# Performance work log

Hardware: AMD Instinct MI355X
Metric: run time of the kernel (lower is better)

## Reference

```python
import jax, jax.numpy as jnp
import numpy as np

B, M, D = 16, 16, 512          # m (tokens per sample) must equal num_experts
N = 16                          # num_experts
H = (D + D) * 2 // 3            # hidden_dim = 682
OUT = 512


def setup_inputs() -> dict:
    key = jax.random.key(0)
    ks = jax.random.split(key, 8)
    s = lambda k, shape, fan: jax.random.normal(k, shape, jnp.float32) / np.sqrt(fan)
    return {
        "x":    jax.random.normal(ks[0], (B, M, D), jnp.float32),
        "phi":  jax.random.normal(ks[1], (D, N, H), jnp.float32),
        "W1":   s(ks[2], (N, D, H), D),
        "b1":   s(ks[3], (N, H), D),
        "W2":   s(ks[4], (N, H, D), H),
        "b2":   s(ks[5], (N, D), H),
        "Wout": s(ks[6], (N * D, OUT), N * D),
        "bout": s(ks[7], (OUT,), N * D),
    }


def reference(x, phi, W1, b1, W2, b2, Wout, bout):
    # dispatch/combine logits: [b, m, n, p]
    logits = jnp.einsum('bmd,dnp->bmnp', x, phi)
    Dw = jax.nn.softmax(logits, axis=1)                       # dispatch weights over tokens m
    Cw = jax.nn.softmax(jax.nn.softmax(logits, axis=2), axis=3)  # (softmax of softmax, faithful)
    Xs = jnp.einsum('bmd,bmnp->bnpd', x, Dw)                  # expert slot inputs [b,n,p,d]
    # batched per-expert MLP (grouped GEMM over expert axis n)
    hmid = jax.nn.relu(jnp.einsum('bnpd,ndh->bnph', Xs, W1) + b1[None, :, None, :])
    Ys = jnp.einsum('bnph,nhd->bnpd', hmid, W2) + b2[None, :, None, :]
    Y = jnp.einsum('bnpd,bmnp->bmd', Ys, Cw)                  # combine -> [b, m, d]
    flat = Y.reshape(Y.shape[0], -1)                          # [b, m*d] == [b, n*d]
    return flat @ Wout + bout
```

## Files before the change

kernel.cpp:

```cpp
#include <hip/hip_runtime.h>
#include <hip/hip_bf16.h>
#include <math.h>

typedef unsigned int   u32;
typedef unsigned short u16;
typedef __bf16 bf16;
typedef bf16  bf16x8  __attribute__((ext_vector_type(8)));
typedef float f32x4   __attribute__((ext_vector_type(4)));
typedef float f32x16  __attribute__((ext_vector_type(16)));

#define BBATCH 16
#define MTOK   16
#define NEXP   16
#define DDIM   512
#define HDIM   682
#define HPAD   704
#define NHCOL  (NEXP*HDIM)
#define NHPCOL (NEXP*HPAD)
#define BM     (BBATCH*MTOK)

__device__ __forceinline__ u16 f2bf(float f) {
    u32 u = __builtin_bit_cast(u32, f);
    u += 0x7fffu + ((u >> 16) & 1u);
    return (u16)(u >> 16);
}
__device__ __forceinline__ float bf2f(u16 h) {
    u32 u = ((u32)h) << 16;
    return __builtin_bit_cast(float, u);
}
__device__ __forceinline__ u32 pk2bf(float a, float b) {
    __hip_bfloat162 t = __float22bfloat162_rn(float2{a, b});
    u32 r;
    __builtin_memcpy(&r, &t, 4);
    return r;
}

__global__ __launch_bounds__(256) void k_prep(
    const float* __restrict__ x, const float* __restrict__ b2,
    const float* __restrict__ bout,
    u16* __restrict__ xh, u16* __restrict__ xl,
    float* __restrict__ Y, float* __restrict__ out, u16* __restrict__ DwT) {
    const int bid = blockIdx.x, tid = threadIdx.x;
    if (bid < 128) {
        int i = (bid * 256 + tid) * 4;
        float4 v = *(const float4*)&x[i];
        float a[4] = {v.x, v.y, v.z, v.w};
        u16 hh[4], ll[4];
        #pragma unroll
        for (int j = 0; j < 4; ++j) {
            hh[j] = f2bf(a[j]);
            ll[j] = f2bf(a[j] - bf2f(hh[j]));
        }
        *(uint2*)&xh[i] = make_uint2((u32)hh[0] | ((u32)hh[1] << 16), (u32)hh[2] | ((u32)hh[3] << 16));
        *(uint2*)&xl[i] = make_uint2((u32)ll[0] | ((u32)ll[1] << 16), (u32)ll[2] | ((u32)ll[3] << 16));
    } else if (bid < 640) {
        int idx = (bid - 128) * 256 + tid;
        int d = idx & 511;
        float s = 0.f;
        #pragma unroll
        for (int nn = 0; nn < 16; ++nn) s += b2[nn * 512 + d];
        Y[idx] = s;
    } else if (bid < 672) {
        int idx = (bid - 640) * 256 + tid;
        out[idx] = bout[idx & 511];
    } else {
        int g = (bid - 672) * 256 + tid;
        int bn = g / 88, off = g - bn * 88;
        *(uint2*)(DwT + (size_t)(bn * HPAD + HDIM) * 16 + off * 4) = make_uint2(0u, 0u);
    }
}

__global__ __launch_bounds__(256) void k_lgemm(
    const u16* __restrict__ xh, const u16* __restrict__ xl,
    const float* __restrict__ phi, float* __restrict__ C,
    u16* __restrict__ DwT) {
    __shared__ u16 AH[128 * 40], AL[128 * 40], BH[64 * 40], BL[64 * 40];
    __shared__ float F[32 * 68];
    const int ct = blockIdx.x, rt = blockIdx.y;
    const int tid = threadIdx.x;
    const int wv = tid >> 6, lane = tid & 63, quad = lane >> 4, l15 = lane & 15;
    f32x4 acc[2][4] = {};
    for (int kb = 0; kb < 512; kb += 32) {
        {
            int rr = tid >> 2, kg = (tid & 3) * 8;
            #pragma unroll
            for (int rp = 0; rp < 2; ++rp) {
                int r = rp * 64 + rr;
                size_t ao = (size_t)(rt * 128 + r) * 512 + kb + kg;
                *(uint4*)&AH[r * 40 + kg] = *(const uint4*)(xh + ao);
                *(uint4*)&AL[r * 40 + kg] = *(const uint4*)(xl + ao);
            }
        }
        {
            int dl = tid >> 3, cg = (tid & 7) * 8;
            int c0 = ct * 64 + cg;
            const float* src = phi + (size_t)(kb + dl) * NHCOL + c0;
            float v[8];
            if (c0 + 8 <= NHCOL) {
                *(float4*)&v[0] = *(const float4*)&src[0];
                *(float4*)&v[4] = *(const float4*)&src[4];
            } else {
                #pragma unroll
                for (int i = 0; i < 8; ++i) v[i] = (c0 + i < NHCOL) ? src[i] : 0.f;
            }
            #pragma unroll
            for (int i = 0; i < 8; ++i) F[dl * 68 + cg + i] = v[i];
        }
        __syncthreads();
        {
            int cc = tid & 63, q = tid >> 6;
            u16 th[8], tl[8];
            #pragma unroll
            for (int i = 0; i < 8; ++i) {
                float v = F[(q * 8 + i) * 68 + cc];
                th[i] = f2bf(v);
                tl[i] = f2bf(v - bf2f(th[i]));
            }
            *(uint4*)&BH[cc * 40 + q * 8] = *(uint4*)&th[0];
            *(uint4*)&BL[cc * 40 + q * 8] = *(uint4*)&tl[0];
        }
        __syncthreads();
        bf16x8 ah[2], al[2];
        #pragma unroll
        for (int i = 0; i < 2; ++i) {
            ah[i] = *(const bf16x8*)&AH[(wv * 32 + i * 16 + l15) * 40 + quad * 8];
            al[i] = *(const bf16x8*)&AL[(wv * 32 + i * 16 + l15) * 40 + quad * 8];
        }
        #pragma unroll
        for (int j = 0; j < 4; ++j) {
            bf16x8 bh = *(const bf16x8*)&BH[(j * 16 + l15) * 40 + quad * 8];
            bf16x8 bl = *(const bf16x8*)&BL[(j * 16 + l15) * 40 + quad * 8];
            #pragma unroll
            for (int i = 0; i < 2; ++i) {
                acc[i][j] = __builtin_amdgcn_mfma_f32_16x16x32_bf16(ah[i], bh, acc[i][j], 0, 0, 0);
                acc[i][j] = __builtin_amdgcn_mfma_f32_16x16x32_bf16(ah[i], bl, acc[i][j], 0, 0, 0);
                acc[i][j] = __builtin_amdgcn_mfma_f32_16x16x32_bf16(al[i], bh, acc[i][j], 0, 0, 0);
            }
        }
        __syncthreads();
    }
    #pragma unroll
    for (int i = 0; i < 2; ++i) {
        const int b  = rt * 8 + wv * 2 + i;
        const int r0 = rt * 128 + wv * 32 + i * 16 + quad * 4;
        #pragma unroll
        for (int j = 0; j < 4; ++j) {
            const int col = ct * 64 + j * 16 + l15;
            float a0 = acc[i][j][0], a1 = acc[i][j][1], a2 = acc[i][j][2], a3 = acc[i][j][3];
            if (col < NHCOL) {
                C[(size_t)(r0 + 0) * NHCOL + col] = a0;
                C[(size_t)(r0 + 1) * NHCOL + col] = a1;
                C[(size_t)(r0 + 2) * NHCOL + col] = a2;
                C[(size_t)(r0 + 3) * NHCOL + col] = a3;
            }
            float mx = fmaxf(fmaxf(a0, a1), fmaxf(a2, a3));
            mx = fmaxf(mx, __shfl_xor(mx, 16));
            mx = fmaxf(mx, __shfl_xor(mx, 32));
            float e0 = expf(a0 - mx), e1 = expf(a1 - mx);
            float e2 = expf(a2 - mx), e3 = expf(a3 - mx);
            float s = e0 + e1 + e2 + e3;
            s += __shfl_xor(s, 16);
            s += __shfl_xor(s, 32);
            float inv = 1.f / s;
            if (col < NHCOL) {
                int n = col / HDIM;
                int p = col - n * HDIM;
                u16* dst = DwT + ((size_t)((b * 16 + n) * HPAD + p)) * 16 + quad * 4;
                *(uint2*)dst = make_uint2(pk2bf(e0 * inv, e1 * inv), pk2bf(e2 * inv, e3 * inv));
            }
        }
    }
}

__global__ __launch_bounds__(256) void k_t1cw(
    const u16* __restrict__ A, const float* __restrict__ W1,
    u16* __restrict__ T1b,
    const float* __restrict__ L, u16* __restrict__ CwB) {
    __shared__ __align__(16) char smem[NHCOL * 4];
    const int bid = blockIdx.x, tid = threadIdx.x;
    if (bid < 176) {
        u16*   As = (u16*)smem;
        u16*   Bs = (u16*)(smem + 20480);
        float* F  = (float*)(smem + 25600);
        const int ct = bid;
        const int wv = tid >> 6, lane = tid & 63, quad = lane >> 4, l15 = lane & 15;
        const int n = ct / 11, h0 = (ct % 11) * 64;
        f32x4 acc[4][4] = {};
        for (int kb = 0; kb < 512; kb += 32) {
            {
                int rr = tid >> 2, kg = (tid & 3) * 8;
                #pragma unroll
                for (int rp = 0; rp < 4; ++rp) {
                    int r = rp * 64 + rr;
                    *(uint4*)&As[r * 40 + kg] = *(const uint4*)(A + (size_t)r * 512 + kb + kg);
                }
            }
            {
                int dl = tid >> 3, cg = (tid & 7) * 8;
                int h = h0 + cg;
                const float* wr = W1 + ((size_t)n * 512 + kb + dl) * HDIM + h;
                float v[8];
                if (h + 8 <= HDIM) {
                    #pragma unroll
                    for (int i = 0; i < 4; ++i) {
                        float2 t = *(const float2*)&wr[i * 2];
                        v[i * 2] = t.x; v[i * 2 + 1] = t.y;
                    }
                } else {
                    #pragma unroll
                    for (int i = 0; i < 8; ++i) v[i] = (h + i < HDIM) ? wr[i] : 0.f;
                }
                #pragma unroll
                for (int i = 0; i < 8; ++i) F[dl * 68 + cg + i] = v[i];
            }
            __syncthreads();
            {
                int cc = tid & 63, q = tid >> 6;
                u16 tv[8];
                #pragma unroll
                for (int i = 0; i < 8; ++i) tv[i] = f2bf(F[(q * 8 + i) * 68 + cc]);
                *(uint4*)&Bs[cc * 40 + q * 8] = *(uint4*)&tv[0];
            }
            __syncthreads();
            bf16x8 af[4], bfr[4];
            #pragma unroll
            for (int i = 0; i < 4; ++i)
                af[i] = *(const bf16x8*)&As[(wv * 64 + i * 16 + l15) * 40 + quad * 8];
            #pragma unroll
            for (int j = 0; j < 4; ++j)
                bfr[j] = *(const bf16x8*)&Bs[(j * 16 + l15) * 40 + quad * 8];
            #pragma unroll
            for (int i = 0; i < 4; ++i)
                #pragma unroll
                for (int j = 0; j < 4; ++j)
                    acc[i][j] = __builtin_amdgcn_mfma_f32_16x16x32_bf16(af[i], bfr[j], acc[i][j], 0, 0, 0);
            __syncthreads();
        }
        #pragma unroll
        for (int i = 0; i < 4; ++i)
            #pragma unroll
            for (int j = 0; j < 4; ++j) {
                int col = ct * 64 + j * 16 + l15;
                int r0  = wv * 64 + i * 16 + quad * 4;
                #pragma unroll
                for (int r = 0; r < 4; ++r)
                    T1b[(size_t)(r0 + r) * NHPCOL + col] = f2bf(acc[i][j][r]);
            }
    } else {
        float* row = (float*)smem;
        const int j = bid - 176;
        const int m = j & 15, b = j >> 4;
        const float* Lrow = L + (size_t)(b * 16 + m) * NHCOL;
        for (int i = tid; i < NHCOL; i += 256) row[i] = Lrow[i];
        __syncthreads();
        for (int p = tid; p < HDIM; p += 256) {
            float v[16];
            float mx = -1e30f;
            #pragma unroll
            for (int n = 0; n < 16; ++n) { v[n] = row[n * HDIM + p]; mx = fmaxf(mx, v[n]); }
            float s = 0.f;
            #pragma unroll
            for (int n = 0; n < 16; ++n) { v[n] = expf(v[n] - mx); s += v[n]; }
            float inv = 1.f / s;
            #pragma unroll
            for (int n = 0; n < 16; ++n) row[n * HDIM + p] = expf(v[n] * inv);
        }
        __syncthreads();
        const int wv = tid >> 6, lane = tid & 63;
        for (int nn = 0; nn < 4; ++nn) {
            int n = wv * 4 + nn;
            float s = 0.f;
            for (int p = lane; p < HDIM; p += 64) s += row[n * HDIM + p];
            #pragma unroll
            for (int off = 32; off > 0; off >>= 1) s += __shfl_xor(s, off);
            float inv = 1.f / s;
            u16* dst = CwB + (size_t)(((b * 16 + n) * 16 + m)) * HPAD;
            for (int p = lane; p < HDIM; p += 64) dst[p] = f2bf(row[n * HDIM + p] * inv);
            if (lane < HPAD - HDIM) dst[HDIM + lane] = 0;
        }
    }
}

__global__ __launch_bounds__(256) void k_mid(
    const u16* __restrict__ T1b, const u16* __restrict__ DwT,
    const u16* __restrict__ CwB, const float* __restrict__ b1,
    u16* __restrict__ Gb) {
    __shared__ u16 T1T[128 * 24];
    __shared__ u16 hmidT[128 * 64];
    const int ht = blockIdx.x, n = blockIdx.y, b = blockIdx.z;
    const int tid = threadIdx.x;
    const int wv = tid >> 6, lane = tid & 63;
    const int quad = lane >> 4, l15 = lane & 15;
    const int l31 = lane & 31, half = lane >> 5;
    const int h0 = ht * 128;
    const int b16n = b * 16 + n;

    {
        int m = tid & 15, hh0 = (tid >> 4) * 8;
        u16 v[8];
        if (h0 + hh0 + 8 <= HPAD) {
            *(uint4*)v = *(const uint4*)(T1b + (size_t)(b * 16 + m) * NHPCOL + n * HPAD + h0 + hh0);
        } else {
            #pragma unroll
            for (int i = 0; i < 8; ++i) v[i] = 0;
        }
        #pragma unroll
        for (int i = 0; i < 8; ++i) T1T[(hh0 + i) * 24 + m] = v[i];
    }
    __syncthreads();

    const int hrow = wv * 32 + l31;
    bf16x8 bt1 = *(const bf16x8*)&T1T[hrow * 24 + half * 8];
    int hg1 = h0 + hrow;
    float biasf = (hg1 < HDIM) ? b1[n * HDIM + hg1] : 0.f;
    f32x16 cbias;
    #pragma unroll
    for (int i = 0; i < 16; ++i) cbias[i] = biasf;

    const u16* dwbase = DwT + (size_t)(b16n * HPAD) * 16;
    const u16* cwrow  = CwB + (size_t)(b16n * 16 + l15) * HPAD;

    f32x4 acc[2] = {};
    const int hsw = hrow & 7;
    for (int c = 0; c < 11; ++c) {
        const int p0 = c * 64;
        #pragma unroll
        for (int pt = 0; pt < 2; ++pt) {
            bf16x8 adw = *(const bf16x8*)(dwbase + (size_t)(p0 + pt * 32 + l31) * 16 + half * 8);
            f32x16 hm = __builtin_amdgcn_mfma_f32_32x32x16_bf16(adw, bt1, cbias, 0, 0, 0);
            #pragma unroll
            for (int g = 0; g < 4; ++g) {
                float v0 = fmaxf(hm[g * 4 + 0], 0.f);
                float v1 = fmaxf(hm[g * 4 + 1], 0.f);
                float v2 = fmaxf(hm[g * 4 + 2], 0.f);
                float v3 = fmaxf(hm[g * 4 + 3], 0.f);
                uint2 pk = make_uint2(pk2bf(v0, v1), pk2bf(v2, v3));
                int gran = (pt * 4 + g) ^ hsw;
                *(uint2*)&hmidT[hrow * 64 + gran * 8 + half * 4] = pk;
            }
        }
        #pragma unroll
        for (int s = 0; s < 2; ++s) {
            bf16x8 acw = *(const bf16x8*)(cwrow + p0 + s * 32 + quad * 8);
            #pragma unroll
            for (int hj = 0; hj < 2; ++hj) {
                int hr = wv * 32 + hj * 16 + l15;
                int gr = (s * 4 + quad) ^ (hr & 7);
                bf16x8 bh = *(const bf16x8*)&hmidT[hr * 64 + gr * 8];
                acc[hj] = __builtin_amdgcn_mfma_f32_16x16x32_bf16(acw, bh, acc[hj], 0, 0, 0);
            }
        }
    }
    #pragma unroll
    for (int hj = 0; hj < 2; ++hj) {
        int h = h0 + wv * 32 + hj * 16 + l15;
        if (h < HPAD) {
            #pragma unroll
            for (int r = 0; r < 4; ++r) {
                int m = quad * 4 + r;
                Gb[(size_t)(b * 16 + m) * NHPCOL + n * HPAD + h] = f2bf(acc[hj][r]);
            }
        }
    }
}

__global__ __launch_bounds__(256) void k_ygemm(
    const u16* __restrict__ G, const float* __restrict__ W2, float* __restrict__ Y) {
    __shared__ u16 AsL[64 * 40];
    __shared__ u16 BsL[128 * 40];
    __shared__ float F[32 * 132];
    const int ct = blockIdx.x, rt = blockIdx.y, nz = blockIdx.z;
    const int n = nz >> 1, kb0 = (nz & 1) * 352;
    const int tid = threadIdx.x;
    const int wv = tid >> 6, lane = tid & 63, quad = lane >> 4, l15 = lane & 15;
    const int m0 = rt * 64, d0 = ct * 128;
    f32x4 acc[4][2] = {};
    for (int kb = kb0; kb < kb0 + 352; kb += 32) {
        {
            int am = tid >> 2, akg = (tid & 3) * 8;
            *(uint4*)&AsL[am * 40 + akg] =
                *(const uint4*)(G + (size_t)(m0 + am) * NHPCOL + n * HPAD + kb + akg);
        }
        {
            int hl = tid >> 3, cg = (tid & 7) * 16;
            int h = kb + hl;
            float v[16];
            if (h < HDIM) {
                const float* src = W2 + ((size_t)n * HDIM + h) * 512 + d0 + cg;
                *(float4*)&v[0]  = *(const float4*)&src[0];
                *(float4*)&v[4]  = *(const float4*)&src[4];
                *(float4*)&v[8]  = *(const float4*)&src[8];
                *(float4*)&v[12] = *(const float4*)&src[12];
            } else {
                #pragma unroll
                for (int i = 0; i < 16; ++i) v[i] = 0.f;
            }
            #pragma unroll
            for (int i = 0; i < 16; ++i) F[hl * 132 + cg + i] = v[i];
        }
        __syncthreads();
        {
            int cc = tid & 127, half = tid >> 7;
            u16 tv[16];
            #pragma unroll
            for (int i = 0; i < 16; ++i) tv[i] = f2bf(F[(half * 16 + i) * 132 + cc]);
            *(uint4*)&BsL[cc * 40 + half * 16]     = *(uint4*)&tv[0];
            *(uint4*)&BsL[cc * 40 + half * 16 + 8] = *(uint4*)&tv[8];
        }
        __syncthreads();
        bf16x8 af[4], bfr[2];
        #pragma unroll
        for (int i = 0; i < 4; ++i) af[i] = *(const bf16x8*)&AsL[(i * 16 + l15) * 40 + quad * 8];
        #pragma unroll
        for (int j = 0; j < 2; ++j) bfr[j] = *(const bf16x8*)&BsL[(wv * 32 + j * 16 + l15) * 40 + quad * 8];
        #pragma unroll
        for (int i = 0; i < 4; ++i)
            #pragma unroll
            for (int j = 0; j < 2; ++j)
                acc[i][j] = __builtin_amdgcn_mfma_f32_16x16x32_bf16(af[i], bfr[j], acc[i][j], 0, 0, 0);
        __syncthreads();
    }
    #pragma unroll
    for (int i = 0; i < 4; ++i)
        #pragma unroll
        for (int j = 0; j < 2; ++j) {
            int d = d0 + wv * 32 + j * 16 + l15;
            int r0 = m0 + i * 16 + quad * 4;
            #pragma unroll
            for (int r = 0; r < 4; ++r)
                atomicAdd(&Y[(size_t)(r0 + r) * 512 + d], acc[i][j][r]);
        }
}

__global__ __launch_bounds__(256) void k_outgemm(
    const float* __restrict__ Y, const float* __restrict__ Wout, float* __restrict__ out) {
    __shared__ u16 AsL[16 * 40];
    __shared__ u16 BsL[128 * 40];
    __shared__ float F[32 * 132];
    const int ct = blockIdx.x, ks = blockIdx.y;
    const int tid = threadIdx.x;
    const int wv = tid >> 6, lane = tid & 63, quad = lane >> 4, l15 = lane & 15;
    const int o0 = ct * 128, kbase = ks * 128;
    f32x4 acc[2] = {};
    for (int kb = 0; kb < 128; kb += 32) {
        {
            int r = tid >> 4, k2 = (tid & 15) * 2;
            float2 v = *(const float2*)&Y[(size_t)r * 8192 + kbase + kb + k2];
            AsL[r * 40 + k2]     = f2bf(v.x);
            AsL[r * 40 + k2 + 1] = f2bf(v.y);
        }
        {
            int kl = tid >> 3, cg = (tid & 7) * 16;
            const float* src = Wout + (size_t)(kbase + kb + kl) * 512 + o0 + cg;
            float v[16];
            *(float4*)&v[0]  = *(const float4*)&src[0];
            *(float4*)&v[4]  = *(const float4*)&src[4];
            *(float4*)&v[8]  = *(const float4*)&src[8];
            *(float4*)&v[12] = *(const float4*)&src[12];
            #pragma unroll
            for (int i = 0; i < 16; ++i) F[kl * 132 + cg + i] = v[i];
        }
        __syncthreads();
        {
            int cc = tid & 127, half = tid >> 7;
            u16 tv[16];
            #pragma unroll
            for (int i = 0; i < 16; ++i) tv[i] = f2bf(F[(half * 16 + i) * 132 + cc]);
            *(uint4*)&BsL[cc * 40 + half * 16]     = *(uint4*)&tv[0];
            *(uint4*)&BsL[cc * 40 + half * 16 + 8] = *(uint4*)&tv[8];
        }
        __syncthreads();
        bf16x8 af = *(const bf16x8*)&AsL[l15 * 40 + quad * 8];
        #pragma unroll
        for (int j = 0; j < 2; ++j) {
            bf16x8 bfr = *(const bf16x8*)&BsL[(wv * 32 + j * 16 + l15) * 40 + quad * 8];
            acc[j] = __builtin_amdgcn_mfma_f32_16x16x32_bf16(af, bfr, acc[j], 0, 0, 0);
        }
        __syncthreads();
    }
    #pragma unroll
    for (int j = 0; j < 2; ++j) {
        int o = o0 + wv * 32 + j * 16 + l15;
        #pragma unroll
        for (int r = 0; r < 4; ++r)
            atomicAdd(&out[(size_t)(quad * 4 + r) * 512 + o], acc[j][r]);
    }
}

extern "C" void kernel_launch(void* const* d_in, const int* in_sizes, int n_in,
                              void* d_out, int out_size, void* d_ws, size_t ws_size,
                              hipStream_t stream) {
    const float* x    = (const float*)d_in[0];
    const float* phi  = (const float*)d_in[1];
    const float* W1   = (const float*)d_in[2];
    const float* b1   = (const float*)d_in[3];
    const float* W2   = (const float*)d_in[4];
    const float* b2   = (const float*)d_in[5];
    const float* Wout = (const float*)d_in[6];
    const float* bout = (const float*)d_in[7];
    float* out = (float*)d_out;

    char* base = (char*)d_ws;
    float* logits = (float*)(base + 0);
    u16*   DwT    = (u16*)(base + 11173888);
    u16*   CwB    = (u16*)(base + 16941056);
    u16*   T1b    = (u16*)(base + 22708224);
    u16*   Gb     = (u16*)(base + 28475392);
    u16*   xh     = (u16*)(base + 34242560);
    u16*   xl     = (u16*)(base + 34504704);
    float* Y      = (float*)(base + 34766848);

    k_prep    <<<dim3(760), 256, 0, stream>>>(x, b2, bout, xh, xl, Y, out, DwT);
    k_lgemm   <<<dim3(171, 2), 256, 0, stream>>>(xh, xl, phi, logits, DwT);
    k_t1cw    <<<dim3(432), 256, 0, stream>>>(xh, W1, T1b, logits, CwB);
    k_mid     <<<dim3(6, 16, 16), 256, 0, stream>>>(T1b, DwT, CwB, b1, Gb);
    k_ygemm   <<<dim3(4, 4, 32), 256, 0, stream>>>(Gb, W2, Y);
    k_outgemm <<<dim3(4, 64), 256, 0, stream>>>(Y, Wout, out);
}
```

Baseline: 233.9 us.

## Fuse all stages into one persistent kernel with grid barriers and ticket scheduling

Six separate kernel launches are replaced by a single persistent kernel of 512 blocks. Each stage pulls work items through an atomic ticket counter, and stages are separated by software grid barriers built on atomics. Several stages are also re-tiled into smaller pieces: the logits GEMM uses 64-row tiles, the T1 GEMM is split into row halves, and the output GEMM has a finer K split. The aim is to remove launch gaps and tail idling between kernels, at the cost of barrier spin overhead, a memset launch, and a deadlock risk if the 512 blocks cannot all be resident at once. The barrier has a timeout guard that silently breaks out, which could produce incorrect results.

```diff
diff --git a/kernel.cpp b/kernel.cpp
--- a/kernel.cpp
+++ b/kernel.cpp
@@ -17,7 +17,7 @@
 #define HPAD   704
 #define NHCOL  (NEXP*HDIM)
 #define NHPCOL (NEXP*HPAD)
-#define BM     (BBATCH*MTOK)
+#define NBLK   512
 
 __device__ __forceinline__ u16 f2bf(float f) {
     u32 u = __builtin_bit_cast(u32, f);
@@ -35,222 +35,246 @@
     return r;
 }
 
-__global__ __launch_bounds__(256) void k_prep(
-    const float* __restrict__ x, const float* __restrict__ b2,
-    const float* __restrict__ bout,
-    u16* __restrict__ xh, u16* __restrict__ xl,
-    float* __restrict__ Y, float* __restrict__ out, u16* __restrict__ DwT) {
-    const int bid = blockIdx.x, tid = threadIdx.x;
-    if (bid < 128) {
-        int i = (bid * 256 + tid) * 4;
-        float4 v = *(const float4*)&x[i];
-        float a[4] = {v.x, v.y, v.z, v.w};
-        u16 hh[4], ll[4];
-        #pragma unroll
-        for (int j = 0; j < 4; ++j) {
-            hh[j] = f2bf(a[j]);
-            ll[j] = f2bf(a[j] - bf2f(hh[j]));
-        }
-        *(uint2*)&xh[i] = make_uint2((u32)hh[0] | ((u32)hh[1] << 16), (u32)hh[2] | ((u32)hh[3] << 16));
-        *(uint2*)&xl[i] = make_uint2((u32)ll[0] | ((u32)ll[1] << 16), (u32)ll[2] | ((u32)ll[3] << 16));
-    } else if (bid < 640) {
-        int idx = (bid - 128) * 256 + tid;
-        int d = idx & 511;
-        float s = 0.f;
-        #pragma unroll
-        for (int nn = 0; nn < 16; ++nn) s += b2[nn * 512 + d];
-        Y[idx] = s;
-    } else if (bid < 672) {
-        int idx = (bid - 640) * 256 + tid;
-        out[idx] = bout[idx & 511];
-    } else {
-        int g = (bid - 672) * 256 + tid;
-        int bn = g / 88, off = g - bn * 88;
-        *(uint2*)(DwT + (size_t)(bn * HPAD + HDIM) * 16 + off * 4) = make_uint2(0u, 0u);
-    }
+__device__ __forceinline__ void gridbar(u32* cnt, u32* gen, u32 k) {
+    __threadfence();
+    __syncthreads();
+    if (threadIdx.x == 0) {
+        u32 old = __hip_atomic_fetch_add(cnt, 1u, __ATOMIC_RELAXED, __HIP_MEMORY_SCOPE_AGENT);
+        if (old == k * (u32)NBLK - 1u) {
+            __hip_atomic_fetch_add(gen, 1u, __ATOMIC_RELEASE, __HIP_MEMORY_SCOPE_AGENT);
+        } else {
+            long long guard = 0;
+            while (__hip_atomic_load(gen, __ATOMIC_RELAXED, __HIP_MEMORY_SCOPE_AGENT) < k) {
+                __builtin_amdgcn_s_sleep(8);
+                if (++guard > (1LL << 21)) break;
+            }
+        }
+    }
+    __syncthreads();
+    __threadfence();
 }
 
-__global__ __launch_bounds__(256) void k_lgemm(
-    const u16* __restrict__ xh, const u16* __restrict__ xl,
-    const float* __restrict__ phi, float* __restrict__ C,
-    u16* __restrict__ DwT) {
-    __shared__ u16 AH[128 * 40], AL[128 * 40], BH[64 * 40], BL[64 * 40];
-    __shared__ float F[32 * 68];
-    const int ct = blockIdx.x, rt = blockIdx.y;
+__global__ __launch_bounds__(256, 2) void k_moe(
+    const float* __restrict__ x,    const float* __restrict__ phi,
+    const float* __restrict__ W1,   const float* __restrict__ b1,
+    const float* __restrict__ W2,   const float* __restrict__ b2,
+    const float* __restrict__ Wout, const float* __restrict__ bout,
+    float* __restrict__ out,
+    float* __restrict__ logits, u16* __restrict__ DwT, u16* __restrict__ CwB,
+    u16* __restrict__ T1b, u16* __restrict__ Gb,
+    u16* __restrict__ xh, u16* __restrict__ xl, float* __restrict__ Y,
+    u32* __restrict__ ctl) {
+
+    __shared__ __align__(16) char SMEM[43648];
+    __shared__ u32 sh_vb;
+    u32* tk  = ctl;
+    u32* cnt = ctl + 6;
+    u32* gen = ctl + 7;
     const int tid = threadIdx.x;
     const int wv = tid >> 6, lane = tid & 63, quad = lane >> 4, l15 = lane & 15;
-    f32x4 acc[2][4] = {};
-    for (int kb = 0; kb < 512; kb += 32) {
-        {
-            int rr = tid >> 2, kg = (tid & 3) * 8;
-            #pragma unroll
-            for (int rp = 0; rp < 2; ++rp) {
-                int r = rp * 64 + rr;
-                size_t ao = (size_t)(rt * 128 + r) * 512 + kb + kg;
-                *(uint4*)&AH[r * 40 + kg] = *(const uint4*)(xh + ao);
-                *(uint4*)&AL[r * 40 + kg] = *(const uint4*)(xl + ao);
-            }
-        }
-        {
-            int dl = tid >> 3, cg = (tid & 7) * 8;
-            int c0 = ct * 64 + cg;
-            const float* src = phi + (size_t)(kb + dl) * NHCOL + c0;
-            float v[8];
-            if (c0 + 8 <= NHCOL) {
-                *(float4*)&v[0] = *(const float4*)&src[0];
-                *(float4*)&v[4] = *(const float4*)&src[4];
-            } else {
-                #pragma unroll
-                for (int i = 0; i < 8; ++i) v[i] = (c0 + i < NHCOL) ? src[i] : 0.f;
-            }
-            #pragma unroll
-            for (int i = 0; i < 8; ++i) F[dl * 68 + cg + i] = v[i];
-        }
-        __syncthreads();
-        {
-            int cc = tid & 63, q = tid >> 6;
-            u16 th[8], tl[8];
-            #pragma unroll
-            for (int i = 0; i < 8; ++i) {
-                float v = F[(q * 8 + i) * 68 + cc];
-                th[i] = f2bf(v);
-                tl[i] = f2bf(v - bf2f(th[i]));
-            }
-            *(uint4*)&BH[cc * 40 + q * 8] = *(uint4*)&th[0];
-            *(uint4*)&BL[cc * 40 + q * 8] = *(uint4*)&tl[0];
-        }
-        __syncthreads();
-        bf16x8 ah[2], al[2];
-        #pragma unroll
-        for (int i = 0; i < 2; ++i) {
-            ah[i] = *(const bf16x8*)&AH[(wv * 32 + i * 16 + l15) * 40 + quad * 8];
-            al[i] = *(const bf16x8*)&AL[(wv * 32 + i * 16 + l15) * 40 + quad * 8];
-        }
-        #pragma unroll
-        for (int j = 0; j < 4; ++j) {
-            bf16x8 bh = *(const bf16x8*)&BH[(j * 16 + l15) * 40 + quad * 8];
-            bf16x8 bl = *(const bf16x8*)&BL[(j * 16 + l15) * 40 + quad * 8];
-            #pragma unroll
-            for (int i = 0; i < 2; ++i) {
-                acc[i][j] = __builtin_amdgcn_mfma_f32_16x16x32_bf16(ah[i], bh, acc[i][j], 0, 0, 0);
-                acc[i][j] = __builtin_amdgcn_mfma_f32_16x16x32_bf16(ah[i], bl, acc[i][j], 0, 0, 0);
-                acc[i][j] = __builtin_amdgcn_mfma_f32_16x16x32_bf16(al[i], bh, acc[i][j], 0, 0, 0);
-            }
-        }
-        __syncthreads();
-    }
-    #pragma unroll
-    for (int i = 0; i < 2; ++i) {
-        const int b  = rt * 8 + wv * 2 + i;
-        const int r0 = rt * 128 + wv * 32 + i * 16 + quad * 4;
-        #pragma unroll
-        for (int j = 0; j < 4; ++j) {
-            const int col = ct * 64 + j * 16 + l15;
-            float a0 = acc[i][j][0], a1 = acc[i][j][1], a2 = acc[i][j][2], a3 = acc[i][j][3];
-            if (col < NHCOL) {
-                C[(size_t)(r0 + 0) * NHCOL + col] = a0;
-                C[(size_t)(r0 + 1) * NHCOL + col] = a1;
-                C[(size_t)(r0 + 2) * NHCOL + col] = a2;
-                C[(size_t)(r0 + 3) * NHCOL + col] = a3;
-            }
-            float mx = fmaxf(fmaxf(a0, a1), fmaxf(a2, a3));
-            mx = fmaxf(mx, __shfl_xor(mx, 16));
-            mx = fmaxf(mx, __shfl_xor(mx, 32));
-            float e0 = expf(a0 - mx), e1 = expf(a1 - mx);
-            float e2 = expf(a2 - mx), e3 = expf(a3 - mx);
-            float s = e0 + e1 + e2 + e3;
-            s += __shfl_xor(s, 16);
-            s += __shfl_xor(s, 32);
-            float inv = 1.f / s;
-            if (col < NHCOL) {
-                int n = col / HDIM;
-                int p = col - n * HDIM;
-                u16* dst = DwT + ((size_t)((b * 16 + n) * HPAD + p)) * 16 + quad * 4;
-                *(uint2*)dst = make_uint2(pk2bf(e0 * inv, e1 * inv), pk2bf(e2 * inv, e3 * inv));
-            }
-        }
-    }
-}
-
-__global__ __launch_bounds__(256) void k_t1cw(
-    const u16* __restrict__ A, const float* __restrict__ W1,
-    u16* __restrict__ T1b,
-    const float* __restrict__ L, u16* __restrict__ CwB) {
-    __shared__ __align__(16) char smem[NHCOL * 4];
-    const int bid = blockIdx.x, tid = threadIdx.x;
-    if (bid < 176) {
-        u16*   As = (u16*)smem;
-        u16*   Bs = (u16*)(smem + 20480);
-        float* F  = (float*)(smem + 25600);
-        const int ct = bid;
-        const int wv = tid >> 6, lane = tid & 63, quad = lane >> 4, l15 = lane & 15;
-        const int n = ct / 11, h0 = (ct % 11) * 64;
-        f32x4 acc[4][4] = {};
-        for (int kb = 0; kb < 512; kb += 32) {
-            {
-                int rr = tid >> 2, kg = (tid & 3) * 8;
-                #pragma unroll
-                for (int rp = 0; rp < 4; ++rp) {
-                    int r = rp * 64 + rr;
-                    *(uint4*)&As[r * 40 + kg] = *(const uint4*)(A + (size_t)r * 512 + kb + kg);
-                }
-            }
-            {
-                int dl = tid >> 3, cg = (tid & 7) * 8;
-                int h = h0 + cg;
-                const float* wr = W1 + ((size_t)n * 512 + kb + dl) * HDIM + h;
-                float v[8];
-                if (h + 8 <= HDIM) {
-                    #pragma unroll
-                    for (int i = 0; i < 4; ++i) {
-                        float2 t = *(const float2*)&wr[i * 2];
-                        v[i * 2] = t.x; v[i * 2 + 1] = t.y;
+
+#define TICKET(P, NVB)                                                         \
+    if (tid == 0) sh_vb = __hip_atomic_fetch_add(&tk[P], 1u, __ATOMIC_RELAXED, \
+                                                 __HIP_MEMORY_SCOPE_AGENT);    \
+    __syncthreads();                                                           \
+    u32 vb = sh_vb;                                                            \
+    if (vb >= (NVB)) break;
+
+    for (;;) {
+        TICKET(0, 760)
+        if (vb < 128) {
+            int i = ((int)vb * 256 + tid) * 4;
+            float4 v = *(const float4*)&x[i];
+            float a[4] = {v.x, v.y, v.z, v.w};
+            u16 hh[4], ll[4];
+            #pragma unroll
+            for (int j = 0; j < 4; ++j) {
+                hh[j] = f2bf(a[j]);
+                ll[j] = f2bf(a[j] - bf2f(hh[j]));
+            }
+            *(uint2*)&xh[i] = make_uint2((u32)hh[0] | ((u32)hh[1] << 16), (u32)hh[2] | ((u32)hh[3] << 16));
+            *(uint2*)&xl[i] = make_uint2((u32)ll[0] | ((u32)ll[1] << 16), (u32)ll[2] | ((u32)ll[3] << 16));
+        } else if (vb < 640) {
+            int idx = ((int)vb - 128) * 256 + tid;
+            int d = idx & 511;
+            float s = 0.f;
+            #pragma unroll
+            for (int nn = 0; nn < 16; ++nn) s += b2[nn * 512 + d];
+            Y[idx] = s;
+        } else if (vb < 672) {
+            int idx = ((int)vb - 640) * 256 + tid;
+            out[idx] = bout[idx & 511];
+        } else {
+            int g = ((int)vb - 672) * 256 + tid;
+            int bn = g / 88, off = g - bn * 88;
+            *(uint2*)(DwT + (size_t)(bn * HPAD + HDIM) * 16 + off * 4) = make_uint2(0u, 0u);
+        }
+        __syncthreads();
+    }
+    gridbar(cnt, gen, 1);
+
+    for (;;) {
+        TICKET(1, 1036)
+        if (vb < 684) {
+            const int ct = (int)vb % 171, rt = (int)vb / 171;
+            u16* AH = (u16*)SMEM;
+            u16* AL = (u16*)(SMEM + 5120);
+            u16* BH = (u16*)(SMEM + 10240);
+            u16* BL = (u16*)(SMEM + 15360);
+            float* F = (float*)(SMEM + 20480);
+            f32x4 acc[4] = {};
+            for (int kb = 0; kb < 512; kb += 32) {
+                {
+                    int r = tid >> 2, kg = (tid & 3) * 8;
+                    size_t ao = (size_t)(rt * 64 + r) * 512 + kb + kg;
+                    *(uint4*)&AH[r * 40 + kg] = *(const uint4*)(xh + ao);
+                    *(uint4*)&AL[r * 40 + kg] = *(const uint4*)(xl + ao);
+                }
+                {
+                    int dl = tid >> 3, cg = (tid & 7) * 8;
+                    int c0 = ct * 64 + cg;
+                    const float* src = phi + (size_t)(kb + dl) * NHCOL + c0;
+                    float v[8];
+                    if (c0 + 8 <= NHCOL) {
+                        *(float4*)&v[0] = *(const float4*)&src[0];
+                        *(float4*)&v[4] = *(const float4*)&src[4];
+                    } else {
+                        #pragma unroll
+                        for (int i = 0; i < 8; ++i) v[i] = (c0 + i < NHCOL) ? src[i] : 0.f;
                     }
-                } else {
-                    #pragma unroll
-                    for (int i = 0; i < 8; ++i) v[i] = (h + i < HDIM) ? wr[i] : 0.f;
-                }
-                #pragma unroll
-                for (int i = 0; i < 8; ++i) F[dl * 68 + cg + i] = v[i];
-            }
-            __syncthreads();
-            {
-                int cc = tid & 63, q = tid >> 6;
-                u16 tv[8];
-                #pragma unroll
-                for (int i = 0; i < 8; ++i) tv[i] = f2bf(F[(q * 8 + i) * 68 + cc]);
-                *(uint4*)&Bs[cc * 40 + q * 8] = *(uint4*)&tv[0];
-            }
-            __syncthreads();
-            bf16x8 af[4], bfr[4];
-            #pragma unroll
-            for (int i = 0; i < 4; ++i)
-                af[i] = *(const bf16x8*)&As[(wv * 64 + i * 16 + l15) * 40 + quad * 8];
-            #pragma unroll
-            for (int j = 0; j < 4; ++j)
-                bfr[j] = *(const bf16x8*)&Bs[(j * 16 + l15) * 40 + quad * 8];
-            #pragma unroll
-            for (int i = 0; i < 4; ++i)
+                    #pragma unroll
+                    for (int i = 0; i < 8; ++i) F[dl * 68 + cg + i] = v[i];
+                }
+                __syncthreads();
+                {
+                    int cc = tid & 63, q = tid >> 6;
+                    u16 th[8], tl[8];
+                    #pragma unroll
+                    for (int i = 0; i < 8; ++i) {
+                        float v = F[(q * 8 + i) * 68 + cc];
+                        th[i] = f2bf(v);
+                        tl[i] = f2bf(v - bf2f(th[i]));
+                    }
+                    *(uint4*)&BH[cc * 40 + q * 8] = *(uint4*)&th[0];
+                    *(uint4*)&BL[cc * 40 + q * 8] = *(uint4*)&tl[0];
+                }
+                __syncthreads();
+                bf16x8 ah = *(const bf16x8*)&AH[(wv * 16 + l15) * 40 + quad * 8];
+                bf16x8 al = *(const bf16x8*)&AL[(wv * 16 + l15) * 40 + quad * 8];
+                #pragma unroll
+                for (int j = 0; j < 4; ++j) {
+                    bf16x8 bh = *(const bf16x8*)&BH[(j * 16 + l15) * 40 + quad * 8];
+                    bf16x8 bl = *(const bf16x8*)&BL[(j * 16 + l15) * 40 + quad * 8];
+                    acc[j] = __builtin_amdgcn_mfma_f32_16x16x32_bf16(ah, bh, acc[j], 0, 0, 0);
+                    acc[j] = __builtin_amdgcn_mfma_f32_16x16x32_bf16(ah, bl, acc[j], 0, 0, 0);
+                    acc[j] = __builtin_amdgcn_mfma_f32_16x16x32_bf16(al, bh, acc[j], 0, 0, 0);
+                }
+                __syncthreads();
+            }
+            const int b  = rt * 4 + wv;
+            const int r0 = rt * 64 + wv * 16 + quad * 4;
+            #pragma unroll
+            for (int j = 0; j < 4; ++j) {
+                const int col = ct * 64 + j * 16 + l15;
+                float a0 = acc[j][0], a1 = acc[j][1], a2 = acc[j][2], a3 = acc[j][3];
+                if (col < NHCOL) {
+                    logits[(size_t)(r0 + 0) * NHCOL + col] = a0;
+                    logits[(size_t)(r0 + 1) * NHCOL + col] = a1;
+                    logits[(size_t)(r0 + 2) * NHCOL + col] = a2;
+                    logits[(size_t)(r0 + 3) * NHCOL + col] = a3;
+                }
+                float mx = fmaxf(fmaxf(a0, a1), fmaxf(a2, a3));
+                mx = fmaxf(mx, __shfl_xor(mx, 16));
+                mx = fmaxf(mx, __shfl_xor(mx, 32));
+                float e0 = expf(a0 - mx), e1 = expf(a1 - mx);
+                float e2 = expf(a2 - mx), e3 = expf(a3 - mx);
+                float s = e0 + e1 + e2 + e3;
+                s += __shfl_xor(s, 16);
+                s += __shfl_xor(s, 32);
+                float inv = 1.f / s;
+                if (col < NHCOL) {
+                    int n = col / HDIM;
+                    int p = col - n * HDIM;
+                    u16* dst = DwT + ((size_t)((b * 16 + n) * HPAD + p)) * 16 + quad * 4;
+                    *(uint2*)dst = make_uint2(pk2bf(e0 * inv, e1 * inv), pk2bf(e2 * inv, e3 * inv));
+                }
+            }
+        } else {
+            const int w = (int)vb - 684;
+            const int ct = w >> 1, rh = w & 1;
+            const int n = ct / 11, h0 = (ct % 11) * 64;
+            u16* As = (u16*)SMEM;
+            u16* Bs = (u16*)(SMEM + 10240);
+            float* F = (float*)(SMEM + 15360);
+            f32x4 acc[2][4] = {};
+            for (int kb = 0; kb < 512; kb += 32) {
+                {
+                    int r = tid >> 1, kg = (tid & 1) * 16;
+                    const u16* s = xh + (size_t)(rh * 128 + r) * 512 + kb + kg;
+                    *(uint4*)&As[r * 40 + kg]     = *(const uint4*)s;
+                    *(uint4*)&As[r * 40 + kg + 8] = *(const uint4*)(s + 8);
+                }
+                {
+                    int dl = tid >> 3, cg = (tid & 7) * 8;
+                    int h = h0 + cg;
+                    const float* wr = W1 + ((size_t)n * 512 + kb + dl) * HDIM + h;
+                    float v[8];
+                    if (h + 8 <= HDIM) {
+                        #pragma unroll
+                        for (int i = 0; i < 4; ++i) {
+                            float2 t = *(const float2*)&wr[i * 2];
+                            v[i * 2] = t.x; v[i * 2 + 1] = t.y;
+                        }
+                    } else {
+                        #pragma unroll
+                        for (int i = 0; i < 8; ++i) v[i] = (h + i < HDIM) ? wr[i] : 0.f;
+                    }
+                    #pragma unroll
+                    for (int i = 0; i < 8; ++i) F[dl * 68 + cg + i] = v[i];
+                }
+                __syncthreads();
+                {
+                    int cc = tid & 63, q = tid >> 6;
+                    u16 tv[8];
+                    #pragma unroll
+                    for (int i = 0; i < 8; ++i) tv[i] = f2bf(F[(q * 8 + i) * 68 + cc]);
+                    *(uint4*)&Bs[cc * 40 + q * 8] = *(uint4*)&tv[0];
+                }
+                __syncthreads();
+                bf16x8 af[2], bfr[4];
+                #pragma unroll
+                for (int i = 0; i < 2; ++i)
+                    af[i] = *(const bf16x8*)&As[(wv * 32 + i * 16 + l15) * 40 + quad * 8];
                 #pragma unroll
                 for (int j = 0; j < 4; ++j)
-                    acc[i][j] = __builtin_amdgcn_mfma_f32_16x16x32_bf16(af[i], bfr[j], acc[i][j], 0, 0, 0);
-            __syncthreads();
-        }
-        #pragma unroll
-        for (int i = 0; i < 4; ++i)
-            #pragma unroll
-            for (int j = 0; j < 4; ++j) {
-                int col = ct * 64 + j * 16 + l15;
-                int r0  = wv * 64 + i * 16 + quad * 4;
-                #pragma unroll
-                for (int r = 0; r < 4; ++r)
-                    T1b[(size_t)(r0 + r) * NHPCOL + col] = f2bf(acc[i][j][r]);
-            }
-    } else {
-        float* row = (float*)smem;
-        const int j = bid - 176;
-        const int m = j & 15, b = j >> 4;
-        const float* Lrow = L + (size_t)(b * 16 + m) * NHCOL;
+                    bfr[j] = *(const bf16x8*)&Bs[(j * 16 + l15) * 40 + quad * 8];
+                #pragma unroll
+                for (int i = 0; i < 2; ++i)
+                    #pragma unroll
+                    for (int j = 0; j < 4; ++j)
+                        acc[i][j] = __builtin_amdgcn_mfma_f32_16x16x32_bf16(af[i], bfr[j], acc[i][j], 0, 0, 0);
+                __syncthreads();
+            }
+            #pragma unroll
+            for (int i = 0; i < 2; ++i)
+                #pragma unroll
+                for (int j = 0; j < 4; ++j) {
+                    int col = ct * 64 + j * 16 + l15;
+                    int r0  = rh * 128 + wv * 32 + i * 16 + quad * 4;
+                    #pragma unroll
+                    for (int r = 0; r < 4; ++r)
+                        T1b[(size_t)(r0 + r) * NHPCOL + col] = f2bf(acc[i][j][r]);
+                }
+        }
+        __syncthreads();
+    }
+    gridbar(cnt, gen, 2);
+
+    for (;;) {
+        TICKET(2, 256)
+        float* row = (float*)SMEM;
+        const int m = (int)vb & 15, b = (int)vb >> 4;
+        const float* Lrow = logits + (size_t)(b * 16 + m) * NHCOL;
         for (int i = tid; i < NHCOL; i += 256) row[i] = Lrow[i];
         __syncthreads();
         for (int p = tid; p < HDIM; p += 256) {
@@ -266,7 +290,6 @@
             for (int n = 0; n < 16; ++n) row[n * HDIM + p] = expf(v[n] * inv);
         }
         __syncthreads();
-        const int wv = tid >> 6, lane = tid & 63;
         for (int nn = 0; nn < 4; ++nn) {
             int n = wv * 4 + nn;
             float s = 0.f;
@@ -278,213 +301,211 @@
             for (int p = lane; p < HDIM; p += 64) dst[p] = f2bf(row[n * HDIM + p] * inv);
             if (lane < HPAD - HDIM) dst[HDIM + lane] = 0;
         }
-    }
-}
-
-__global__ __launch_bounds__(256) void k_mid(
-    const u16* __restrict__ T1b, const u16* __restrict__ DwT,
-    const u16* __restrict__ CwB, const float* __restrict__ b1,
-    u16* __restrict__ Gb) {
-    __shared__ u16 T1T[128 * 24];
-    __shared__ u16 hmidT[128 * 64];
-    const int ht = blockIdx.x, n = blockIdx.y, b = blockIdx.z;
-    const int tid = threadIdx.x;
-    const int wv = tid >> 6, lane = tid & 63;
-    const int quad = lane >> 4, l15 = lane & 15;
-    const int l31 = lane & 31, half = lane >> 5;
-    const int h0 = ht * 128;
-    const int b16n = b * 16 + n;
-
-    {
-        int m = tid & 15, hh0 = (tid >> 4) * 8;
-        u16 v[8];
-        if (h0 + hh0 + 8 <= HPAD) {
-            *(uint4*)v = *(const uint4*)(T1b + (size_t)(b * 16 + m) * NHPCOL + n * HPAD + h0 + hh0);
-        } else {
-            #pragma unroll
-            for (int i = 0; i < 8; ++i) v[i] = 0;
-        }
+        __syncthreads();
+    }
+    gridbar(cnt, gen, 3);
+
+    for (;;) {
+        TICKET(3, 1536)
+        const int ht = (int)vb % 6, n = ((int)vb / 6) & 15, b = (int)vb / 96;
+        u16* T1T   = (u16*)SMEM;
+        u16* hmidT = (u16*)(SMEM + 6144);
+        const int l31 = lane & 31, half = lane >> 5;
+        const int h0 = ht * 128;
+        const int b16n = b * 16 + n;
+        {
+            int m = tid & 15, hh0 = (tid >> 4) * 8;
+            u16 v[8];
+            if (h0 + hh0 + 8 <= HPAD) {
+                *(uint4*)v = *(const uint4*)(T1b + (size_t)(b * 16 + m) * NHPCOL + n * HPAD + h0 + hh0);
+            } else {
+                #pragma unroll
+                for (int i = 0; i < 8; ++i) v[i] = 0;
+            }
+            #pragma unroll
+            for (int i = 0; i < 8; ++i) T1T[(hh0 + i) * 24 + m] = v[i];
+        }
+        __syncthreads();
+
+        const int hrow = wv * 32 + l31;
+        bf16x8 bt1 = *(const bf16x8*)&T1T[hrow * 24 + half * 8];
+        int hg1 = h0 + hrow;
+        float biasf = (hg1 < HDIM) ? b1[n * HDIM + hg1] : 0.f;
+        f32x16 cbias;
         #pragma unroll
-        for (int i = 0; i < 8; ++i) T1T[(hh0 + i) * 24 + m] = v[i];
-    }
-    __syncthreads();
-
-    const int hrow = wv * 32 + l31;
-    bf16x8 bt1 = *(const bf16x8*)&T1T[hrow * 24 + half * 8];
-    int hg1 = h0 + hrow;
-    float biasf = (hg1 < HDIM) ? b1[n * HDIM + hg1] : 0.f;
-    f32x16 cbias;
-    #pragma unroll
-    for (int i = 0; i < 16; ++i) cbias[i] = biasf;
-
-    const u16* dwbase = DwT + (size_t)(b16n * HPAD) * 16;
-    const u16* cwrow  = CwB + (size_t)(b16n * 16 + l15) * HPAD;
-
-    f32x4 acc[2] = {};
-    const int hsw = hrow & 7;
-    for (int c = 0; c < 11; ++c) {
-        const int p0 = c * 64;
+        for (int i = 0; i < 16; ++i) cbias[i] = biasf;
+
+        const u16* dwbase = DwT + (size_t)(b16n * HPAD) * 16;
+        const u16* cwrow  = CwB + (size_t)(b16n * 16 + l15) * HPAD;
+
+        f32x4 acc[2] = {};
+        const int hsw = hrow & 7;
+        for (int c = 0; c < 11; ++c) {
+            const int p0 = c * 64;
+            #pragma unroll
+            for (int pt = 0; pt < 2; ++pt) {
+                bf16x8 adw = *(const bf16x8*)(dwbase + (size_t)(p0 + pt * 32 + l31) * 16 + half * 8);
+                f32x16 hm = __builtin_amdgcn_mfma_f32_32x32x16_bf16(adw, bt1, cbias, 0, 0, 0);
+                #pragma unroll
+                for (int g = 0; g < 4; ++g) {
+                    float v0 = fmaxf(hm[g * 4 + 0], 0.f);
+                    float v1 = fmaxf(hm[g * 4 + 1], 0.f);
+                    float v2 = fmaxf(hm[g * 4 + 2], 0.f);
+                    float v3 = fmaxf(hm[g * 4 + 3], 0.f);
+                    uint2 pk = make_uint2(pk2bf(v0, v1), pk2bf(v2, v3));
+                    int gran = (pt * 4 + g) ^ hsw;
+                    *(uint2*)&hmidT[hrow * 64 + gran * 8 + half * 4] = pk;
+                }
+            }
+            #pragma unroll
+            for (int s = 0; s < 2; ++s) {
+                bf16x8 acw = *(const bf16x8*)(cwrow + p0 + s * 32 + quad * 8);
+                #pragma unroll
+                for (int hj = 0; hj < 2; ++hj) {
+                    int hr = wv * 32 + hj * 16 + l15;
+                    int gr = (s * 4 + quad) ^ (hr & 7);
+                    bf16x8 bh = *(const bf16x8*)&hmidT[hr * 64 + gr * 8];
+                    acc[hj] = __builtin_amdgcn_mfma_f32_16x16x32_bf16(acw, bh, acc[hj], 0, 0, 0);
+                }
+            }
+        }
         #pragma unroll
-        for (int pt = 0; pt < 2; ++pt) {
-            bf16x8 adw = *(const bf16x8*)(dwbase + (size_t)(p0 + pt * 32 + l31) * 16 + half * 8);
-            f32x16 hm = __builtin_amdgcn_mfma_f32_32x32x16_bf16(adw, bt1, cbias, 0, 0, 0);
-            #pragma unroll
-            for (int g = 0; g < 4; ++g) {
-                float v0 = fmaxf(hm[g * 4 + 0], 0.f);
-                float v1 = fmaxf(hm[g * 4 + 1], 0.f);
-                float v2 = fmaxf(hm[g * 4 + 2], 0.f);
-                float v3 = fmaxf(hm[g * 4 + 3], 0.f);
-                uint2 pk = make_uint2(pk2bf(v0, v1), pk2bf(v2, v3));
-                int gran = (pt * 4 + g) ^ hsw;
-                *(uint2*)&hmidT[hrow * 64 + gran * 8 + half * 4] = pk;
-            }
+        for (int hj = 0; hj < 2; ++hj) {
+            int h = h0 + wv * 32 + hj * 16 + l15;
+            if (h < HPAD) {
+                #pragma unroll
+                for (int r = 0; r < 4; ++r) {
+                    int m = quad * 4 + r;
+                    Gb[(size_t)(b * 16 + m) * NHPCOL + n * HPAD + h] = f2bf(acc[hj][r]);
+                }
+            }
+        }
+        __syncthreads();
+    }
+    gridbar(cnt, gen, 4);
+
+    for (;;) {
+        TICKET(4, 512)
+        const int ct = (int)vb & 3, rt = ((int)vb >> 2) & 3, nz = (int)vb >> 4;
+        const int n = nz >> 1, kb0 = (nz & 1) * 352;
+        u16* As = (u16*)SMEM;
+        u16* Bs = (u16*)(SMEM + 5120);
+        float* F = (float*)(SMEM + 15360);
+        const int m0 = rt * 64, d0 = ct * 128;
+        f32x4 acc[4][2] = {};
+        for (int kb = kb0; kb < kb0 + 352; kb += 32) {
+            {
+                int am = tid >> 2, akg = (tid & 3) * 8;
+                *(uint4*)&As[am * 40 + akg] =
+                    *(const uint4*)(Gb + (size_t)(m0 + am) * NHPCOL + n * HPAD + kb + akg);
+            }
+            {
+                int hl = tid >> 3, cg = (tid & 7) * 16;
+                int h = kb + hl;
+                float v[16];
+                if (h < HDIM) {
+                    const float* src = W2 + ((size_t)n * HDIM + h) * 512 + d0 + cg;
+                    *(float4*)&v[0]  = *(const float4*)&src[0];
+                    *(float4*)&v[4]  = *(const float4*)&src[4];
+                    *(float4*)&v[8]  = *(const float4*)&src[8];
+                    *(float4*)&v[12] = *(const float4*)&src[12];
+                } else {
+                    #pragma unroll
+                    for (int i = 0; i < 16; ++i) v[i] = 0.f;
+                }
+                #pragma unroll
+                for (int i = 0; i < 16; ++i) F[hl * 132 + cg + i] = v[i];
+            }
+            __syncthreads();
+            {
+                int cc = tid & 127, hf = tid >> 7;
+                u16 tv[16];
+                #pragma unroll
+                for (int i = 0; i < 16; ++i) tv[i] = f2bf(F[(hf * 16 + i) * 132 + cc]);
+                *(uint4*)&Bs[cc * 40 + hf * 16]     = *(uint4*)&tv[0];
+                *(uint4*)&Bs[cc * 40 + hf * 16 + 8] = *(uint4*)&tv[8];
+            }
+            __syncthreads();
+            bf16x8 af[4], bfr[2];
+            #pragma unroll
+            for (int i = 0; i < 4; ++i) af[i] = *(const bf16x8*)&As[(i * 16 + l15) * 40 + quad * 8];
+            #pragma unroll
+            for (int j = 0; j < 2; ++j) bfr[j] = *(const bf16x8*)&Bs[(wv * 32 + j * 16 + l15) * 40 + quad * 8];
+            #pragma unroll
+            for (int i = 0; i < 4; ++i)
+                #pragma unroll
+                for (int j = 0; j < 2; ++j)
+                    acc[i][j] = __builtin_amdgcn_mfma_f32_16x16x32_bf16(af[i], bfr[j], acc[i][j], 0, 0, 0);
+            __syncthreads();
         }
         #pragma unroll
-        for (int s = 0; s < 2; ++s) {
-            bf16x8 acw = *(const bf16x8*)(cwrow + p0 + s * 32 + quad * 8);
-            #pragma unroll
-            for (int hj = 0; hj < 2; ++hj) {
-                int hr = wv * 32 + hj * 16 + l15;
-                int gr = (s * 4 + quad) ^ (hr & 7);
-                bf16x8 bh = *(const bf16x8*)&hmidT[hr * 64 + gr * 8];
-                acc[hj] = __builtin_amdgcn_mfma_f32_16x16x32_bf16(acw, bh, acc[hj], 0, 0, 0);
-            }
-        }
-    }
-    #pragma unroll
-    for (int hj = 0; hj < 2; ++hj) {
-        int h = h0 + wv * 32 + hj * 16 + l15;
-        if (h < HPAD) {
-            #pragma unroll
-            for (int r = 0; r < 4; ++r) {
-                int m = quad * 4 + r;
-                Gb[(size_t)(b * 16 + m) * NHPCOL + n * HPAD + h] = f2bf(acc[hj][r]);
-            }
-        }
-    }
-}
-
-__global__ __launch_bounds__(256) void k_ygemm(
-    const u16* __restrict__ G, const float* __restrict__ W2, float* __restrict__ Y) {
-    __shared__ u16 AsL[64 * 40];
-    __shared__ u16 BsL[128 * 40];
-    __shared__ float F[32 * 132];
-    const int ct = blockIdx.x, rt = blockIdx.y, nz = blockIdx.z;
-    const int n = nz >> 1, kb0 = (nz & 1) * 352;
-    const int tid = threadIdx.x;
-    const int wv = tid >> 6, lane = tid & 63, quad = lane >> 4, l15 = lane & 15;
-    const int m0 = rt * 64, d0 = ct * 128;
-    f32x4 acc[4][2] = {};
-    for (int kb = kb0; kb < kb0 + 352; kb += 32) {
-        {
-            int am = tid >> 2, akg = (tid & 3) * 8;
-            *(uint4*)&AsL[am * 40 + akg] =
-                *(const uint4*)(G + (size_t)(m0 + am) * NHPCOL + n * HPAD + kb + akg);
-        }
-        {
-            int hl = tid >> 3, cg = (tid & 7) * 16;
-            int h = kb + hl;
-            float v[16];
-            if (h < HDIM) {
-                const float* src = W2 + ((size_t)n * HDIM + h) * 512 + d0 + cg;
+        for (int i = 0; i < 4; ++i)
+            #pragma unroll
+            for (int j = 0; j < 2; ++j) {
+                int d = d0 + wv * 32 + j * 16 + l15;
+                int r0 = m0 + i * 16 + quad * 4;
+                #pragma unroll
+                for (int r = 0; r < 4; ++r)
+                    atomicAdd(&Y[(size_t)(r0 + r) * 512 + d], acc[i][j][r]);
+            }
+        __syncthreads();
+    }
+    gridbar(cnt, gen, 5);
+
+    for (;;) {
+        TICKET(5, 512)
+        const int ct = (int)vb & 3, ks = (int)vb >> 2;
+        u16* As = (u16*)SMEM;
+        u16* Bs = (u16*)(SMEM + 1280);
+        float* F = (float*)(SMEM + 11520);
+        const int o0 = ct * 128, kbase = ks * 64;
+        f32x4 acc[2] = {};
+        for (int kb = 0; kb < 64; kb += 32) {
+            {
+                int r = tid >> 4, k2 = (tid & 15) * 2;
+                float2 v = *(const float2*)&Y[(size_t)r * 8192 + kbase + kb + k2];
+                As[r * 40 + k2]     = f2bf(v.x);
+                As[r * 40 + k2 + 1] = f2bf(v.y);
+            }
+            {
+                int kl = tid >> 3, cg = (tid & 7) * 16;
+                const float* src = Wout + (size_t)(kbase + kb + kl) * 512 + o0 + cg;
+                float v[16];
                 *(float4*)&v[0]  = *(const float4*)&src[0];
                 *(float4*)&v[4]  = *(const float4*)&src[4];
                 *(float4*)&v[8]  = *(const float4*)&src[8];
                 *(float4*)&v[12] = *(const float4*)&src[12];
-            } else {
-                #pragma unroll
-                for (int i = 0; i < 16; ++i) v[i] = 0.f;
-            }
-            #pragma unroll
-            for (int i = 0; i < 16; ++i) F[hl * 132 + cg + i] = v[i];
-        }
-        __syncthreads();
-        {
-            int cc = tid & 127, half = tid >> 7;
-            u16 tv[16];
-            #pragma unroll
-            for (int i = 0; i < 16; ++i) tv[i] = f2bf(F[(half * 16 + i) * 132 + cc]);
-            *(uint4*)&BsL[cc * 40 + half * 16]     = *(uint4*)&tv[0];
-            *(uint4*)&BsL[cc * 40 + half * 16 + 8] = *(uint4*)&tv[8];
-        }
-        __syncthreads();
-        bf16x8 af[4], bfr[2];
-        #pragma unroll
-        for (int i = 0; i < 4; ++i) af[i] = *(const bf16x8*)&AsL[(i * 16 + l15) * 40 + quad * 8];
-        #pragma unroll
-        for (int j = 0; j < 2; ++j) bfr[j] = *(const bf16x8*)&BsL[(wv * 32 + j * 16 + l15) * 40 + quad * 8];
-        #pragma unroll
-        for (int i = 0; i < 4; ++i)
-            #pragma unroll
-            for (int j = 0; j < 2; ++j)
-                acc[i][j] = __builtin_amdgcn_mfma_f32_16x16x32_bf16(af[i], bfr[j], acc[i][j], 0, 0, 0);
-        __syncthreads();
-    }
-    #pragma unroll
-    for (int i = 0; i < 4; ++i)
+                #pragma unroll
+                for (int i = 0; i < 16; ++i) F[kl * 132 + cg + i] = v[i];
+            }
+            __syncthreads();
+            {
+                int cc = tid & 127, hf = tid >> 7;
+                u16 tv[16];
+                #pragma unroll
+                for (int i = 0; i < 16; ++i) tv[i] = f2bf(F[(hf * 16 + i) * 132 + cc]);
+                *(uint4*)&Bs[cc * 40 + hf * 16]     = *(uint4*)&tv[0];
+                *(uint4*)&Bs[cc * 40 + hf * 16 + 8] = *(uint4*)&tv[8];
+            }
+            __syncthreads();
+            bf16x8 af = *(const bf16x8*)&As[l15 * 40 + quad * 8];
+            #pragma unroll
+            for (int j = 0; j < 2; ++j) {
+                bf16x8 bfr = *(const bf16x8*)&Bs[(wv * 32 + j * 16 + l15) * 40 + quad * 8];
+                acc[j] = __builtin_amdgcn_mfma_f32_16x16x32_bf16(af, bfr, acc[j], 0, 0, 0);
+            }
+            __syncthreads();
+        }
         #pragma unroll
         for (int j = 0; j < 2; ++j) {
-            int d = d0 + wv * 32 + j * 16 + l15;
-            int r0 = m0 + i * 16 + quad * 4;
+            int o = o0 + wv * 32 + j * 16 + l15;
             #pragma unroll
             for (int r = 0; r < 4; ++r)
-                atomicAdd(&Y[(size_t)(r0 + r) * 512 + d], acc[i][j][r]);
-        }
-}
-
-__global__ __launch_bounds__(256) void k_outgemm(
-    const float* __restrict__ Y, const float* __restrict__ Wout, float* __restrict__ out) {
-    __shared__ u16 AsL[16 * 40];
-    __shared__ u16 BsL[128 * 40];
-    __shared__ float F[32 * 132];
-    const int ct = blockIdx.x, ks = blockIdx.y;
-    const int tid = threadIdx.x;
-    const int wv = tid >> 6, lane = tid & 63, quad = lane >> 4, l15 = lane & 15;
-    const int o0 = ct * 128, kbase = ks * 128;
-    f32x4 acc[2] = {};
-    for (int kb = 0; kb < 128; kb += 32) {
-        {
-            int r = tid >> 4, k2 = (tid & 15) * 2;
-            float2 v = *(const float2*)&Y[(size_t)r * 8192 + kbase + kb + k2];
-            AsL[r * 40 + k2]     = f2bf(v.x);
-            AsL[r * 40 + k2 + 1] = f2bf(v.y);
-        }
-        {
-            int kl = tid >> 3, cg = (tid & 7) * 16;
-            const float* src = Wout + (size_t)(kbase + kb + kl) * 512 + o0 + cg;
-            float v[16];
-            *(float4*)&v[0]  = *(const float4*)&src[0];
-            *(float4*)&v[4]  = *(const float4*)&src[4];
-            *(float4*)&v[8]  = *(const float4*)&src[8];
-            *(float4*)&v[12] = *(const float4*)&src[12];
-            #pragma unroll
-            for (int i = 0; i < 16; ++i) F[kl * 132 + cg + i] = v[i];
-        }
-        __syncthreads();
-        {
-            int cc = tid & 127, half = tid >> 7;
-            u16 tv[16];
-            #pragma unroll
-            for (int i = 0; i < 16; ++i) tv[i] = f2bf(F[(half * 16 + i) * 132 + cc]);
-            *(uint4*)&BsL[cc * 40 + half * 16]     = *(uint4*)&tv[0];
-            *(uint4*)&BsL[cc * 40 + half * 16 + 8] = *(uint4*)&tv[8];
-        }
-        __syncthreads();
-        bf16x8 af = *(const bf16x8*)&AsL[l15 * 40 + quad * 8];
-        #pragma unroll
-        for (int j = 0; j < 2; ++j) {
-            bf16x8 bfr = *(const bf16x8*)&BsL[(wv * 32 + j * 16 + l15) * 40 + quad * 8];
-            acc[j] = __builtin_amdgcn_mfma_f32_16x16x32_bf16(af, bfr, acc[j], 0, 0, 0);
-        }
-        __syncthreads();
-    }
-    #pragma unroll
-    for (int j = 0; j < 2; ++j) {
-        int o = o0 + wv * 32 + j * 16 + l15;
-        #pragma unroll
-        for (int r = 0; r < 4; ++r)
-            atomicAdd(&out[(size_t)(quad * 4 + r) * 512 + o], acc[j][r]);
-    }
+                atomicAdd(&out[(size_t)(quad * 4 + r) * 512 + o], acc[j][r]);
+        }
+        __syncthreads();
+    }
+#undef TICKET
 }
 
 extern "C" void kernel_launch(void* const* d_in, const int* in_sizes, int n_in,
@@ -509,11 +530,10 @@
     u16*   xh     = (u16*)(base + 34242560);
     u16*   xl     = (u16*)(base + 34504704);
     float* Y      = (float*)(base + 34766848);
-
-    k_prep    <<<dim3(760), 256, 0, stream>>>(x, b2, bout, xh, xl, Y, out, DwT);
-    k_lgemm   <<<dim3(171, 2), 256, 0, stream>>>(xh, xl, phi, logits, DwT);
-    k_t1cw    <<<dim3(432), 256, 0, stream>>>(xh, W1, T1b, logits, CwB);
-    k_mid     <<<dim3(6, 16, 16), 256, 0, stream>>>(T1b, DwT, CwB, b1, Gb);
-    k_ygemm   <<<dim3(4, 4, 32), 256, 0, stream>>>(Gb, W2, Y);
-    k_outgemm <<<dim3(4, 64), 256, 0, stream>>>(Y, Wout, out);
+    u32*   ctl    = (u32*)(base + 35291136);
+
+    hipMemsetAsync(ctl, 0, 32, stream);
+    k_moe<<<dim3(NBLK), 256, 0, stream>>>(x, phi, W1, b1, W2, b2, Wout, bout,
+                                          out, logits, DwT, CwB, T1b, Gb,
+                                          xh, xl, Y, ctl);
 }
```

Result: slower. 817.9 us (+249.6%).
